# Optimization experiments

Hardware: AMD Instinct MI355X
Metric: run time of the kernel (lower is better)

The kernel has to match this reference:

```python
import jax, jax.numpy as jnp
import numpy as np

N, G, E = 100000, 32768, 1000000
F, H = 64, 64


def _mlp(x, w1, b1, w2, b2):
    # Linear -> SiLU -> Linear (matches nn.Sequential in the torch module)
    return jax.nn.silu(x @ w1 + b1) @ w2 + b2


def setup_inputs() -> dict:
    key = jax.random.key(0)
    ks = jax.random.split(key, 24)

    def lin(k, fan_in, fan_out):
        s = 1.0 / np.sqrt(fan_in)
        kw, kb = jax.random.split(k)
        w = jax.random.uniform(kw, (fan_in, fan_out), jnp.float32, -s, s)
        b = jax.random.uniform(kb, (fan_out,), jnp.float32, -s, s)
        return w, b

    node_w1, node_b1 = lin(ks[0], F, H)
    node_w2, node_b2 = lin(ks[1], H, H)
    edge_w1, edge_b1 = lin(ks[2], 6, H)
    edge_w2, edge_b2 = lin(ks[3], H, H)
    msg_w1, msg_b1 = lin(ks[4], 2 * H, H)
    msg_w2, msg_b2 = lin(ks[5], H, H)
    upd_w1, upd_b1 = lin(ks[6], H, H)
    upd_w2, upd_b2 = lin(ks[7], H, H)

    return {
        "node_features": jax.random.normal(ks[8], (N, F), jnp.float32),
        "node_pos": jax.random.normal(ks[9], (N, 3), jnp.float32),
        "grid_pos": jax.random.normal(ks[10], (G, 3), jnp.float32),
        "orientations": jax.random.normal(ks[11], (N, 3, 3), jnp.float32),
        "edge_index": jnp.stack([
            jax.random.randint(ks[12], (E,), 0, N),
            jax.random.randint(ks[13], (E,), 0, G),
        ]),
        "node_w1": node_w1, "node_b1": node_b1, "node_w2": node_w2, "node_b2": node_b2,
        "edge_w1": edge_w1, "edge_b1": edge_b1, "edge_w2": edge_w2, "edge_b2": edge_b2,
        "msg_w1": msg_w1, "msg_b1": msg_b1, "msg_w2": msg_w2, "msg_b2": msg_b2,
        "upd_w1": upd_w1, "upd_b1": upd_b1, "upd_w2": upd_w2, "upd_b2": upd_b2,
    }


def reference(node_features, node_pos, grid_pos, orientations, edge_index,
              node_w1, node_b1, node_w2, node_b2,
              edge_w1, edge_b1, edge_w2, edge_b2,
              msg_w1, msg_b1, msg_w2, msg_b2,
              upd_w1, upd_b1, upd_w2, upd_b2):
    source, target = edge_index[0], edge_index[1]
    num_grid = grid_pos.shape[0]

    # node MLP
    h_node = _mlp(node_features, node_w1, node_b1, node_w2, node_b2)  # [N,H]

    # per-edge message with orientation-aware projection
    pos_s = node_pos[source]                 # [E,3]
    rel = grid_pos[target] - pos_s           # [E,3]
    # bmm(rel[:,None,:], R[source]).squeeze(1) == einsum ei,eij->ej
    trel = jnp.einsum("ei,eij->ej", rel, orientations[source])
    edge_attr = jnp.concatenate([pos_s, trel], axis=-1)        # [E,6]
    e_feat = _mlp(edge_attr, edge_w1, edge_b1, edge_w2, edge_b2)
    msg_in = jnp.concatenate([h_node[source], e_feat], axis=-1)  # [E,2H]
    messages = _mlp(msg_in, msg_w1, msg_b1, msg_w2, msg_b2)      # [E,H]

    # scatter-mean into grid buckets (mask out-of-range targets)
    valid = (target >= 0) & (target < num_grid)
    idx = jnp.where(valid, target, 0)
    msg_masked = jnp.where(valid[:, None], messages, 0.0)
    sums = jax.ops.segment_sum(msg_masked, idx, num_segments=num_grid)
    cnts = jax.ops.segment_sum(valid.astype(jnp.float32), idx, num_segments=num_grid)
    grid_feat = sums / jnp.maximum(cnts, 1.0)[:, None]

    return _mlp(grid_feat, upd_w1, upd_b1, upd_w2, upd_b2)  # [G,H]
```

## Files before the change

kernel.cpp:

```cpp
#include <hip/hip_runtime.h>
#include <cstdint>

typedef __attribute__((ext_vector_type(8))) short short8;
typedef __attribute__((ext_vector_type(4))) float f32x4;
typedef unsigned short u16;

__device__ __forceinline__ float b2f(u16 u) {
  union { unsigned int i; float f; } v; v.i = ((unsigned int)u) << 16; return v.f;
}
__device__ __forceinline__ u16 f2b(float f) {
  union { float f; unsigned int i; } v; v.f = f;
  unsigned int x = v.i;
  return (u16)((x + 0x7fffu + ((x >> 16) & 1u)) >> 16);
}
__device__ __forceinline__ float silu_f(float x) { return x / (1.0f + __expf(-x)); }

__device__ __forceinline__ float loadF(const void* p, long i, int isf32) {
  if (isf32) return ((const float*)p)[i];
  return b2f(((const u16*)p)[i]);
}

struct Ptrs { const void* p[20]; int n[20]; };

#define FW_NW1 0
#define FW_NW2 4096
#define FW_UW1 8192
#define FW_UW2 12288
#define FW_EW1 16384
#define FW_NB1 16768
#define FW_NB2 16832
#define FW_UB1 16896
#define FW_UB2 16960
#define FW_EB1 17024
#define FW_EB2 17088
#define FW_MB1 17152
#define FW_MB2 17216
#define FW_TOTAL 17280

#define IMG_EW2 0
#define IMG_MW1 4608
#define IMG_MW2 13312
#define IMG_TOTAL 17920

__global__ __launch_bounds__(256) void detect_k(Ptrs a, int* flags) {
  int j = blockIdx.x;
  const u16* q = (const u16*)a.p[j];
  int n = a.n[j];
  int m = n < 4096 ? n : 4096;
  int cnt = 0;
  for (int i = threadIdx.x; i < m; i += 256) {
    unsigned e = (q[i] >> 7) & 0xffu;
    if (e >= 0xC0u) cnt++;
  }
  __shared__ int tot;
  if (threadIdx.x == 0) tot = 0;
  __syncthreads();
  if (cnt) atomicAdd(&tot, cnt);
  __syncthreads();
  if (threadIdx.x == 0) flags[j] = (tot >= 2) ? 1 : 0;
}

__global__ __launch_bounds__(256) void prep_k(Ptrs a, const int* flags,
                                              u16* img, float* fw) {
  int i = blockIdx.x * 256 + threadIdx.x;
  if (i < IMG_TOTAL) {
    u16 val = 0;
    if (i < IMG_MW1) {
      int nn = i / 72, k = i % 72;
      if (k < 64) val = f2b(loadF(a.p[10], (long)k * 64 + nn, flags[10]));
    } else if (i < IMG_MW2) {
      int t2 = i - IMG_MW1; int nn = t2 / 136, k = t2 % 136;
      if (k < 128) val = f2b(loadF(a.p[12], (long)k * 64 + nn, flags[12]));
    } else {
      int t2 = i - IMG_MW2; int nn = t2 / 72, k = t2 % 72;
      if (k < 64) val = f2b(loadF(a.p[14], (long)k * 64 + nn, flags[14]));
    }
    img[i] = val;
  } else if (i < IMG_TOTAL + FW_TOTAL) {
    int j = i - IMG_TOTAL;
    float v;
    if (j < 4096)            v = loadF(a.p[4],  j,          flags[4]);
    else if (j < 8192)       v = loadF(a.p[6],  j - 4096,   flags[6]);
    else if (j < 12288)      v = loadF(a.p[16], j - 8192,   flags[16]);
    else if (j < 16384)      v = loadF(a.p[18], j - 12288,  flags[18]);
    else if (j < 16768)      v = loadF(a.p[8],  j - 16384,  flags[8]);
    else {
      int b = j - 16768; int seg = b >> 6, c = b & 63;
      const void* bp; int bf;
      switch (seg) {
        case 0: bp = a.p[5];  bf = flags[5];  break;
        case 1: bp = a.p[7];  bf = flags[7];  break;
        case 2: bp = a.p[17]; bf = flags[17]; break;
        case 3: bp = a.p[19]; bf = flags[19]; break;
        case 4: bp = a.p[9];  bf = flags[9];  break;
        case 5: bp = a.p[11]; bf = flags[11]; break;
        case 6: bp = a.p[13]; bf = flags[13]; break;
        default: bp = a.p[15]; bf = flags[15]; break;
      }
      v = loadF(bp, c, bf);
    }
    fw[j] = v;
  }
}

__global__ __launch_bounds__(256) void node_mlp(
    const void* x, const int* flags, const float* fw, u16* out, int nrows)
{
  __shared__ float xs[64][68];
  __shared__ float w1s[64][68];
  __shared__ float w2s[64][68];
  __shared__ float b1s[64];
  __shared__ float b2s[64];
  const int t = threadIdx.x;
  const int xf = flags[0];
  const long rbase = (long)blockIdx.x * 64;
  for (int i = t; i < 4096; i += 256) {
    int k = i >> 6, cc = i & 63;
    w1s[k][cc] = fw[FW_NW1 + i];
    w2s[k][cc] = fw[FW_NW2 + i];
  }
  if (t < 64) { b1s[t] = fw[FW_NB1 + t]; b2s[t] = fw[FW_NB2 + t]; }
  {
    int row = t >> 2, ch = t & 3;
    long rg = rbase + row;
    if (rg < nrows) {
      if (xf) {
        const float* xp = (const float*)x + rg * 64 + ch * 16;
#pragma unroll
        for (int m = 0; m < 16; ++m) xs[row][ch * 16 + m] = xp[m];
      } else {
        const u16* xp = (const u16*)x + rg * 64 + ch * 16;
#pragma unroll
        for (int m = 0; m < 16; ++m) xs[row][ch * 16 + m] = b2f(xp[m]);
      }
    } else {
#pragma unroll
      for (int m = 0; m < 16; ++m) xs[row][ch * 16 + m] = 0.f;
    }
  }
  __syncthreads();
  const int r0 = (t >> 4) * 4, c0 = (t & 15) * 4;
  float acc[4][4];
#pragma unroll
  for (int i = 0; i < 4; ++i)
#pragma unroll
    for (int j = 0; j < 4; ++j) acc[i][j] = b1s[c0 + j];
  for (int k = 0; k < 64; ++k) {
    float w0 = w1s[k][c0], w1v = w1s[k][c0 + 1], w2v = w1s[k][c0 + 2], w3v = w1s[k][c0 + 3];
#pragma unroll
    for (int i = 0; i < 4; ++i) {
      float a = xs[r0 + i][k];
      acc[i][0] = fmaf(a, w0, acc[i][0]);
      acc[i][1] = fmaf(a, w1v, acc[i][1]);
      acc[i][2] = fmaf(a, w2v, acc[i][2]);
      acc[i][3] = fmaf(a, w3v, acc[i][3]);
    }
  }
  __syncthreads();
#pragma unroll
  for (int i = 0; i < 4; ++i)
#pragma unroll
    for (int j = 0; j < 4; ++j) xs[r0 + i][c0 + j] = silu_f(acc[i][j]);
  __syncthreads();
  float acc2[4][4];
#pragma unroll
  for (int i = 0; i < 4; ++i)
#pragma unroll
    for (int j = 0; j < 4; ++j) acc2[i][j] = b2s[c0 + j];
  for (int k = 0; k < 64; ++k) {
    float w0 = w2s[k][c0], w1v = w2s[k][c0 + 1], w2v = w2s[k][c0 + 2], w3v = w2s[k][c0 + 3];
#pragma unroll
    for (int i = 0; i < 4; ++i) {
      float a = xs[r0 + i][k];
      acc2[i][0] = fmaf(a, w0, acc2[i][0]);
      acc2[i][1] = fmaf(a, w1v, acc2[i][1]);
      acc2[i][2] = fmaf(a, w2v, acc2[i][2]);
      acc2[i][3] = fmaf(a, w3v, acc2[i][3]);
    }
  }
#pragma unroll
  for (int i = 0; i < 4; ++i) {
    long rg = rbase + r0 + i;
    if (rg < nrows) {
#pragma unroll
      for (int j = 0; j < 4; ++j) out[rg * 64 + c0 + j] = f2b(acc2[i][j]);
    }
  }
}

#define ETILES 4

__global__ __launch_bounds__(256, 2) void edge_kernel(
    const void* node_pos, const void* grid_pos, const void* orient,
    const int* __restrict__ eidx, const u16* __restrict__ h_node,
    const u16* __restrict__ img, const float* __restrict__ fw,
    const int* __restrict__ flags,
    float* __restrict__ sums, float* __restrict__ counts,
    long E, int G)
{
  __shared__ __align__(16) u16 wTs[IMG_TOTAL];
  __shared__ __align__(16) float eaf[64][8];
  __shared__ __align__(16) u16 hA[64][136];
  __shared__ __align__(16) u16 ef1[64][72];
  __shared__ float w1e[6][64];
  __shared__ float biasE[4][64];
  __shared__ int src_s[64];
  __shared__ int tgt_s[64];

  const int t = threadIdx.x;
  const int pf = flags[1], gf = flags[2], of = flags[3];

  {
    const short8* src = (const short8*)img;
    short8* dst = (short8*)wTs;
#pragma unroll
    for (int it = 0; it < 9; ++it) {
      int idx = t + 256 * it;
      if (idx < IMG_TOTAL / 8) dst[idx] = src[idx];
    }
  }
  for (int i = t; i < 384; i += 256) w1e[i / 64][i % 64] = fw[FW_EW1 + i];
  { int seg = t >> 6, cc = t & 63; biasE[seg][cc] = fw[FW_EB1 + seg * 64 + cc]; }

  const int lane = t & 63, w = t >> 6;
  const int q = lane >> 4, c = lane & 15;
  const int m0 = w * 16;
  const u16* wE2 = &wTs[IMG_EW2];
  const u16* wM1 = &wTs[IMG_MW1];
  const u16* wM2 = &wTs[IMG_MW2];
  const f32x4 z = {0.f, 0.f, 0.f, 0.f};

  for (int tile = 0; tile < ETILES; ++tile) {
    long base = ((long)blockIdx.x * ETILES + tile) * 64;
    if (base >= E) break;
    __syncthreads();
    if (t < 64) {
      long eg = base + t;
      int s, tg;
      if (eg < E) { s = eidx[eg]; tg = eidx[E + eg]; }
      else { s = 0; tg = -1; }
      src_s[t] = s;
      tgt_s[t] = tg;
      bool valid = (tg >= 0) && (tg < G);
      if (valid) unsafeAtomicAdd(counts + tg, 1.0f);
      int tgc = valid ? tg : 0;
      float ps[3], rel[3], tr[3];
#pragma unroll
      for (int i = 0; i < 3; ++i) {
        ps[i] = loadF(node_pos, (long)s * 3 + i, pf);
        rel[i] = loadF(grid_pos, (long)tgc * 3 + i, gf) - ps[i];
      }
#pragma unroll
      for (int j = 0; j < 3; ++j) tr[j] = 0.f;
#pragma unroll
      for (int i = 0; i < 3; ++i)
#pragma unroll
        for (int j = 0; j < 3; ++j)
          tr[j] = fmaf(rel[i], loadF(orient, (long)s * 9 + i * 3 + j, of), tr[j]);
      eaf[t][0] = ps[0]; eaf[t][1] = ps[1]; eaf[t][2] = ps[2];
      eaf[t][3] = tr[0]; eaf[t][4] = tr[1]; eaf[t][5] = tr[2];
    }
    __syncthreads();
    {
      int e = t >> 2, ch = t & 3;
      const u16* hp = h_node + (long)src_s[e] * 64 + ch * 16;
      short8 v0 = *(const short8*)hp;
      short8 v1 = *(const short8*)(hp + 8);
      *(short8*)&hA[e][ch * 16] = v0;
      *(short8*)&hA[e][ch * 16 + 8] = v1;
    }
    __syncthreads();

    {
      int e = t >> 2, c0 = (t & 3) * 16;
      float a0 = eaf[e][0], a1 = eaf[e][1], a2 = eaf[e][2];
      float a3 = eaf[e][3], a4 = eaf[e][4], a5 = eaf[e][5];
      __align__(16) u16 tmp[16];
#pragma unroll
      for (int j = 0; j < 16; ++j) {
        int cc = c0 + j;
        float acc = biasE[0][cc];
        acc = fmaf(a0, w1e[0][cc], acc);
        acc = fmaf(a1, w1e[1][cc], acc);
        acc = fmaf(a2, w1e[2][cc], acc);
        acc = fmaf(a3, w1e[3][cc], acc);
        acc = fmaf(a4, w1e[4][cc], acc);
        acc = fmaf(a5, w1e[5][cc], acc);
        tmp[j] = f2b(silu_f(acc));
      }
      *(short8*)&ef1[e][c0] = *(const short8*)tmp;
      *(short8*)&ef1[e][c0 + 8] = *(const short8*)(tmp + 8);
    }
    __syncthreads();
    {
      short8 a0 = *(const short8*)&ef1[m0 + c][q * 8];
      short8 a1 = *(const short8*)&ef1[m0 + c][32 + q * 8];
#pragma unroll
      for (int nt = 0; nt < 4; ++nt) {
        short8 b0 = *(const short8*)&wE2[(nt * 16 + c) * 72 + q * 8];
        short8 b1v = *(const short8*)&wE2[(nt * 16 + c) * 72 + 32 + q * 8];
        f32x4 acc = __builtin_amdgcn_mfma_f32_16x16x32_bf16(a0, b0, z, 0, 0, 0);
        acc = __builtin_amdgcn_mfma_f32_16x16x32_bf16(a1, b1v, acc, 0, 0, 0);
#pragma unroll
        for (int r = 0; r < 4; ++r) {
          int row = m0 + q * 4 + r, col = nt * 16 + c;
          hA[row][64 + col] = f2b(acc[r] + biasE[1][col]);
        }
      }
    }
    __syncthreads();
    {
      short8 a0 = *(const short8*)&hA[m0 + c][q * 8];
      short8 a1 = *(const short8*)&hA[m0 + c][32 + q * 8];
      short8 a2 = *(const short8*)&hA[m0 + c][64 + q * 8];
      short8 a3 = *(const short8*)&hA[m0 + c][96 + q * 8];
#pragma unroll
      for (int nt = 0; nt < 4; ++nt) {
        const u16* wp = &wM1[(nt * 16 + c) * 136];
        f32x4 acc = __builtin_amdgcn_mfma_f32_16x16x32_bf16(a0, *(const short8*)(wp + q * 8), z, 0, 0, 0);
        acc = __builtin_amdgcn_mfma_f32_16x16x32_bf16(a1, *(const short8*)(wp + 32 + q * 8), acc, 0, 0, 0);
        acc = __builtin_amdgcn_mfma_f32_16x16x32_bf16(a2, *(const short8*)(wp + 64 + q * 8), acc, 0, 0, 0);
        acc = __builtin_amdgcn_mfma_f32_16x16x32_bf16(a3, *(const short8*)(wp + 96 + q * 8), acc, 0, 0, 0);
#pragma unroll
        for (int r = 0; r < 4; ++r) {
          int row = m0 + q * 4 + r, col = nt * 16 + c;
          ef1[row][col] = f2b(silu_f(acc[r] + biasE[2][col]));
        }
      }
    }
    __syncthreads();
    {
      short8 a0 = *(const short8*)&ef1[m0 + c][q * 8];
      short8 a1 = *(const short8*)&ef1[m0 + c][32 + q * 8];
      int rtg[4];
#pragma unroll
      for (int r = 0; r < 4; ++r) rtg[r] = tgt_s[m0 + q * 4 + r];
#pragma unroll
      for (int nt = 0; nt < 4; ++nt) {
        short8 b0 = *(const short8*)&wM2[(nt * 16 + c) * 72 + q * 8];
        short8 b1v = *(const short8*)&wM2[(nt * 16 + c) * 72 + 32 + q * 8];
        f32x4 acc = __builtin_amdgcn_mfma_f32_16x16x32_bf16(a0, b0, z, 0, 0, 0);
        acc = __builtin_amdgcn_mfma_f32_16x16x32_bf16(a1, b1v, acc, 0, 0, 0);
#pragma unroll
        for (int r = 0; r < 4; ++r) {
          int tg = rtg[r];
          if (tg >= 0 && tg < G) {
            int col = nt * 16 + c;
            unsafeAtomicAdd(sums + (long)tg * 64 + col, acc[r] + biasE[3][col]);
          }
        }
      }
    }
  }
}

__global__ __launch_bounds__(256) void upd_mlp(
    const float* __restrict__ sums, const float* __restrict__ counts,
    const float* __restrict__ fw, float* __restrict__ out, int nrows)
{
  __shared__ float xs[64][68];
  __shared__ float w1s[64][68];
  __shared__ float w2s[64][68];
  __shared__ float b1s[64];
  __shared__ float b2s[64];
  const int t = threadIdx.x;
  const long rbase = (long)blockIdx.x * 64;
  for (int i = t; i < 4096; i += 256) {
    int k = i >> 6, cc = i & 63;
    w1s[k][cc] = fw[FW_UW1 + i];
    w2s[k][cc] = fw[FW_UW2 + i];
  }
  if (t < 64) { b1s[t] = fw[FW_UB1 + t]; b2s[t] = fw[FW_UB2 + t]; }
  {
    int row = t >> 2, ch = t & 3;
    long rg = rbase + row;
    if (rg < nrows) {
      float inv = 1.0f / fmaxf(counts[rg], 1.0f);
      const float* p = sums + rg * 64 + ch * 16;
#pragma unroll
      for (int m = 0; m < 16; ++m) xs[row][ch * 16 + m] = p[m] * inv;
    } else {
#pragma unroll
      for (int m = 0; m < 16; ++m) xs[row][ch * 16 + m] = 0.f;
    }
  }
  __syncthreads();
  const int r0 = (t >> 4) * 4, c0 = (t & 15) * 4;
  float acc[4][4];
#pragma unroll
  for (int i = 0; i < 4; ++i)
#pragma unroll
    for (int j = 0; j < 4; ++j) acc[i][j] = b1s[c0 + j];
  for (int k = 0; k < 64; ++k) {
    float w0 = w1s[k][c0], w1v = w1s[k][c0 + 1], w2v = w1s[k][c0 + 2], w3v = w1s[k][c0 + 3];
#pragma unroll
    for (int i = 0; i < 4; ++i) {
      float a = xs[r0 + i][k];
      acc[i][0] = fmaf(a, w0, acc[i][0]);
      acc[i][1] = fmaf(a, w1v, acc[i][1]);
      acc[i][2] = fmaf(a, w2v, acc[i][2]);
      acc[i][3] = fmaf(a, w3v, acc[i][3]);
    }
  }
  __syncthreads();
#pragma unroll
  for (int i = 0; i < 4; ++i)
#pragma unroll
    for (int j = 0; j < 4; ++j) xs[r0 + i][c0 + j] = silu_f(acc[i][j]);
  __syncthreads();
  float acc2[4][4];
#pragma unroll
  for (int i = 0; i < 4; ++i)
#pragma unroll
    for (int j = 0; j < 4; ++j) acc2[i][j] = b2s[c0 + j];
  for (int k = 0; k < 64; ++k) {
    float w0 = w2s[k][c0], w1v = w2s[k][c0 + 1], w2v = w2s[k][c0 + 2], w3v = w2s[k][c0 + 3];
#pragma unroll
    for (int i = 0; i < 4; ++i) {
      float a = xs[r0 + i][k];
      acc2[i][0] = fmaf(a, w0, acc2[i][0]);
      acc2[i][1] = fmaf(a, w1v, acc2[i][1]);
      acc2[i][2] = fmaf(a, w2v, acc2[i][2]);
      acc2[i][3] = fmaf(a, w3v, acc2[i][3]);
    }
  }
#pragma unroll
  for (int i = 0; i < 4; ++i) {
    long rg = rbase + r0 + i;
    if (rg < nrows) {
#pragma unroll
      for (int j = 0; j < 4; ++j) out[rg * 64 + c0 + j] = acc2[i][j];
    }
  }
}

extern "C" void kernel_launch(void* const* d_in, const int* in_sizes, int n_in,
                              void* d_out, int out_size, void* d_ws, size_t ws_size,
                              hipStream_t stream) {
  const int N = in_sizes[1] / 3;
  const int G = in_sizes[2] / 3;
  const long E = (long)in_sizes[4] / 2;

  char* ws = (char*)d_ws;
  int* flags = (int*)ws;
  float* sums = (float*)(ws + 256);
  float* counts = (float*)(ws + 256 + (size_t)G * 256);
  const size_t off_h = 256 + (size_t)G * 256 + (size_t)G * 4;
  u16* h_node = (u16*)(ws + off_h);
  const size_t off_img = off_h + (size_t)N * 128;
  u16* img = (u16*)(ws + off_img);
  const size_t off_fw = off_img + (size_t)IMG_TOTAL * 2;
  float* fw = (float*)(ws + off_fw);

  hipMemsetAsync(ws, 0, off_h, stream);

  Ptrs a;
  const int map[20] = {0,1,2,3, 5,6,7,8, 9,10,11,12, 13,14,15,16, 17,18,19,20};
  for (int i = 0; i < 20; ++i) { a.p[i] = d_in[map[i]]; a.n[i] = in_sizes[map[i]]; }

  detect_k<<<20, 256, 0, stream>>>(a, flags);
  prep_k<<<(IMG_TOTAL + FW_TOTAL + 255) / 256, 256, 0, stream>>>(a, flags, img, fw);
  node_mlp<<<(N + 63) / 64, 256, 0, stream>>>(d_in[0], flags, fw, h_node, N);
  edge_kernel<<<(int)((E + ETILES * 64 - 1) / (ETILES * 64)), 256, 0, stream>>>(
      d_in[1], d_in[2], d_in[3], (const int*)d_in[4], h_node, img, fw, flags,
      sums, counts, E, G);
  upd_mlp<<<(G + 63) / 64, 256, 0, stream>>>(sums, counts, fw, (float*)d_out, G);
}
```

Before: 486.8 us.

## Sort edges by target via counting sort and reduce segments before atomics

Adds a histogram, a single-block exclusive scan and a scatter pass that bucket edges by grid target into packed source/target words. The edge kernel then processes edges in target order and combines runs of equal targets per wavefront in shared memory. Only run boundaries that may be shared with neighbouring wavefronts use atomics; interior runs are written with plain stores. This is meant to remove most of the per-element float atomics into sums. The edge kernel also stops staging the weight image in LDS and reads weights from global memory, which allows higher occupancy. The cost is three extra kernels, including a serial single-block scan over 32768 entries, and the packing assumes node indices fit in 17 bits.

```diff
diff --git a/kernel.cpp b/kernel.cpp
--- a/kernel.cpp
+++ b/kernel.cpp
@@ -103,6 +103,61 @@
   }
 }
 
+__global__ __launch_bounds__(256) void hist_k(const int* __restrict__ eidx,
+                                              int* __restrict__ cnt, long E, int G) {
+  long i = (long)blockIdx.x * 256 + threadIdx.x;
+  const long stride = (long)gridDim.x * 256;
+  for (; i < E; i += stride) {
+    int tg = eidx[E + i];
+    if (tg >= 0 && tg < G) atomicAdd(&cnt[tg], 1);
+  }
+}
+
+__global__ __launch_bounds__(1024) void scan_k(const int* __restrict__ cnt,
+                                               int* __restrict__ cursor,
+                                               int* __restrict__ evp, int G) {
+  __shared__ int sd[1024];
+  __shared__ int carry;
+  const int t = threadIdx.x;
+  if (t == 0) carry = 0;
+  __syncthreads();
+  for (int c0 = 0; c0 < G; c0 += 1024) {
+    int i = c0 + t;
+    int v = (i < G) ? cnt[i] : 0;
+    sd[t] = v;
+    __syncthreads();
+    for (int off = 1; off < 1024; off <<= 1) {
+      int x = (t >= off) ? sd[t - off] : 0;
+      __syncthreads();
+      sd[t] += x;
+      __syncthreads();
+    }
+    int excl = sd[t] - v + carry;
+    if (i < G) cursor[i] = excl;
+    int tot = sd[1023];
+    __syncthreads();
+    if (t == 0) carry += tot;
+    __syncthreads();
+  }
+  if (t == 0) *evp = carry;
+}
+
+__global__ __launch_bounds__(256) void scat_k(const int* __restrict__ eidx,
+                                              int* __restrict__ cursor,
+                                              unsigned int* __restrict__ pkS,
+                                              long E, int G) {
+  long i = (long)blockIdx.x * 256 + threadIdx.x;
+  const long stride = (long)gridDim.x * 256;
+  for (; i < E; i += stride) {
+    int tg = eidx[E + i];
+    if (tg >= 0 && tg < G) {
+      int s = eidx[i];
+      int p = atomicAdd(&cursor[tg], 1);
+      pkS[p] = (unsigned int)s | ((unsigned int)tg << 17);
+    }
+  }
+}
+
 __global__ __launch_bounds__(256) void node_mlp(
     const void* x, const int* flags, const float* fw, u16* out, int nrows)
 {
@@ -190,18 +245,17 @@
 
 #define ETILES 4
 
-__global__ __launch_bounds__(256, 2) void edge_kernel(
+__global__ __launch_bounds__(256, 3) void edge_kernel(
     const void* node_pos, const void* grid_pos, const void* orient,
-    const int* __restrict__ eidx, const u16* __restrict__ h_node,
-    const u16* __restrict__ img, const float* __restrict__ fw,
-    const int* __restrict__ flags,
-    float* __restrict__ sums, float* __restrict__ counts,
-    long E, int G)
+    const unsigned int* __restrict__ pkS, const int* __restrict__ evp,
+    const u16* __restrict__ h_node, const u16* __restrict__ img,
+    const float* __restrict__ fw, const int* __restrict__ flags,
+    float* __restrict__ sums, int G)
 {
-  __shared__ __align__(16) u16 wTs[IMG_TOTAL];
-  __shared__ __align__(16) float eaf[64][8];
   __shared__ __align__(16) u16 hA[64][136];
   __shared__ __align__(16) u16 ef1[64][72];
+  __shared__ __align__(16) float msgf[64][66];
+  __shared__ float eaf[64][6];
   __shared__ float w1e[6][64];
   __shared__ float biasE[4][64];
   __shared__ int src_s[64];
@@ -209,41 +263,34 @@
 
   const int t = threadIdx.x;
   const int pf = flags[1], gf = flags[2], of = flags[3];
-
-  {
-    const short8* src = (const short8*)img;
-    short8* dst = (short8*)wTs;
-#pragma unroll
-    for (int it = 0; it < 9; ++it) {
-      int idx = t + 256 * it;
-      if (idx < IMG_TOTAL / 8) dst[idx] = src[idx];
-    }
-  }
+  const int Ev = *evp;
+
   for (int i = t; i < 384; i += 256) w1e[i / 64][i % 64] = fw[FW_EW1 + i];
   { int seg = t >> 6, cc = t & 63; biasE[seg][cc] = fw[FW_EB1 + seg * 64 + cc]; }
 
   const int lane = t & 63, w = t >> 6;
   const int q = lane >> 4, c = lane & 15;
   const int m0 = w * 16;
-  const u16* wE2 = &wTs[IMG_EW2];
-  const u16* wM1 = &wTs[IMG_MW1];
-  const u16* wM2 = &wTs[IMG_MW2];
+  const u16* wE2 = img + IMG_EW2;
+  const u16* wM1 = img + IMG_MW1;
+  const u16* wM2 = img + IMG_MW2;
   const f32x4 z = {0.f, 0.f, 0.f, 0.f};
 
   for (int tile = 0; tile < ETILES; ++tile) {
     long base = ((long)blockIdx.x * ETILES + tile) * 64;
-    if (base >= E) break;
+    if (base >= Ev) break;
     __syncthreads();
     if (t < 64) {
       long eg = base + t;
       int s, tg;
-      if (eg < E) { s = eidx[eg]; tg = eidx[E + eg]; }
-      else { s = 0; tg = -1; }
+      if (eg < Ev) {
+        unsigned int pk = pkS[eg];
+        s = (int)(pk & 0x1FFFFu);
+        tg = (int)(pk >> 17);
+      } else { s = 0; tg = -1; }
       src_s[t] = s;
       tgt_s[t] = tg;
-      bool valid = (tg >= 0) && (tg < G);
-      if (valid) unsafeAtomicAdd(counts + tg, 1.0f);
-      int tgc = valid ? tg : 0;
+      int tgc = (tg >= 0) ? tg : 0;
       float ps[3], rel[3], tr[3];
 #pragma unroll
       for (int i = 0; i < 3; ++i) {
@@ -332,9 +379,6 @@
     {
       short8 a0 = *(const short8*)&ef1[m0 + c][q * 8];
       short8 a1 = *(const short8*)&ef1[m0 + c][32 + q * 8];
-      int rtg[4];
-#pragma unroll
-      for (int r = 0; r < 4; ++r) rtg[r] = tgt_s[m0 + q * 4 + r];
 #pragma unroll
       for (int nt = 0; nt < 4; ++nt) {
         short8 b0 = *(const short8*)&wM2[(nt * 16 + c) * 72 + q * 8];
@@ -343,19 +387,44 @@
         acc = __builtin_amdgcn_mfma_f32_16x16x32_bf16(a1, b1v, acc, 0, 0, 0);
 #pragma unroll
         for (int r = 0; r < 4; ++r) {
-          int tg = rtg[r];
-          if (tg >= 0 && tg < G) {
-            int col = nt * 16 + c;
-            unsafeAtomicAdd(sums + (long)tg * 64 + col, acc[r] + biasE[3][col]);
+          int row = m0 + q * 4 + r, col = nt * 16 + c;
+          msgf[row][col] = acc[r] + biasE[3][col];
+        }
+      }
+    }
+    __syncthreads();
+    {
+      int col = lane;
+      int r0 = w * 16;
+      int cur = tgt_s[r0];
+      float run = msgf[r0][col];
+      bool lopen = (r0 == 0) ? true : (tgt_s[r0 - 1] == cur);
+#pragma unroll
+      for (int r2 = 1; r2 < 16; ++r2) {
+        int r = r0 + r2;
+        int tg = tgt_s[r];
+        float v = msgf[r][col];
+        if (tg == cur) {
+          run += v;
+        } else {
+          if (cur >= 0) {
+            if (lopen) unsafeAtomicAdd(&sums[(long)cur * 64 + col], run);
+            else sums[(long)cur * 64 + col] = run;
           }
+          cur = tg; run = v; lopen = false;
         }
       }
+      bool ropen = (r0 + 16 >= 64) ? true : (tgt_s[r0 + 16] == cur);
+      if (cur >= 0) {
+        if (lopen || ropen) unsafeAtomicAdd(&sums[(long)cur * 64 + col], run);
+        else sums[(long)cur * 64 + col] = run;
+      }
     }
   }
 }
 
 __global__ __launch_bounds__(256) void upd_mlp(
-    const float* __restrict__ sums, const float* __restrict__ counts,
+    const float* __restrict__ sums, const int* __restrict__ cnt,
     const float* __restrict__ fw, float* __restrict__ out, int nrows)
 {
   __shared__ float xs[64][68];
@@ -375,7 +444,7 @@
     int row = t >> 2, ch = t & 3;
     long rg = rbase + row;
     if (rg < nrows) {
-      float inv = 1.0f / fmaxf(counts[rg], 1.0f);
+      float inv = 1.0f / fmaxf((float)cnt[rg], 1.0f);
       const float* p = sums + rg * 64 + ch * 16;
 #pragma unroll
       for (int m = 0; m < 16; ++m) xs[row][ch * 16 + m] = p[m] * inv;
@@ -443,16 +512,17 @@
 
   char* ws = (char*)d_ws;
   int* flags = (int*)ws;
+  int* evp = flags + 24;
   float* sums = (float*)(ws + 256);
-  float* counts = (float*)(ws + 256 + (size_t)G * 256);
-  const size_t off_h = 256 + (size_t)G * 256 + (size_t)G * 4;
-  u16* h_node = (u16*)(ws + off_h);
-  const size_t off_img = off_h + (size_t)N * 128;
-  u16* img = (u16*)(ws + off_img);
-  const size_t off_fw = off_img + (size_t)IMG_TOTAL * 2;
-  float* fw = (float*)(ws + off_fw);
-
-  hipMemsetAsync(ws, 0, off_h, stream);
+  size_t off = 256 + (size_t)G * 256;
+  int* cnt = (int*)(ws + off);     off += (size_t)G * 4;
+  int* cursor = (int*)(ws + off);  off += (size_t)G * 4;
+  unsigned int* pkS = (unsigned int*)(ws + off); off += (size_t)E * 4;
+  u16* h_node = (u16*)(ws + off);  off += (size_t)N * 128;
+  u16* img = (u16*)(ws + off);     off += (size_t)IMG_TOTAL * 2;
+  float* fw = (float*)(ws + off);
+
+  hipMemsetAsync(ws, 0, 256 + (size_t)G * 256 + (size_t)G * 4, stream);
 
   Ptrs a;
   const int map[20] = {0,1,2,3, 5,6,7,8, 9,10,11,12, 13,14,15,16, 17,18,19,20};
@@ -460,9 +530,12 @@
 
   detect_k<<<20, 256, 0, stream>>>(a, flags);
   prep_k<<<(IMG_TOTAL + FW_TOTAL + 255) / 256, 256, 0, stream>>>(a, flags, img, fw);
+  hist_k<<<1024, 256, 0, stream>>>((const int*)d_in[4], cnt, E, G);
+  scan_k<<<1, 1024, 0, stream>>>(cnt, cursor, evp, G);
   node_mlp<<<(N + 63) / 64, 256, 0, stream>>>(d_in[0], flags, fw, h_node, N);
+  scat_k<<<1024, 256, 0, stream>>>((const int*)d_in[4], cursor, pkS, E, G);
   edge_kernel<<<(int)((E + ETILES * 64 - 1) / (ETILES * 64)), 256, 0, stream>>>(
-      d_in[1], d_in[2], d_in[3], (const int*)d_in[4], h_node, img, fw, flags,
-      sums, counts, E, G);
-  upd_mlp<<<(G + 63) / 64, 256, 0, stream>>>(sums, counts, fw, (float*)d_out, G);
-}
+      d_in[1], d_in[2], d_in[3], pkS, evp, h_node, img, fw, flags,
+      sums, G);
+  upd_mlp<<<(G + 63) / 64, 256, 0, stream>>>(sums, cnt, fw, (float*)d_out, G);
+}
```

Measured after the change: 529.3 us. 8.7% more time.
